# Performance work log

Measured on AMD Instinct MI355X. Metric: run time of the kernel, lower is better.

The kernel has to match this reference:

```python
import jax, jax.numpy as jnp
import numpy as np

NUM_HEADS = 8

def _l2norm(t, eps=1e-12):
    # F.normalize(p=2, dim=-1) with eps clamp
    n = jnp.sqrt(jnp.sum(t * t, axis=-1, keepdims=True))
    return t / jnp.maximum(n, eps)

def setup_inputs() -> dict:
    key = jax.random.key(0)
    ks = jax.random.split(key, 4)
    B, N, C = 16, 3136, 768
    x = jax.random.normal(ks[0], (B, N, C), dtype=jnp.float32)
    W_qkv = jax.random.normal(ks[1], (C, 3 * C), dtype=jnp.float32) * (1.0 / np.sqrt(C))
    temp = jnp.ones((NUM_HEADS, 1, 1), dtype=jnp.float32)
    W_proj = jax.random.normal(ks[2], (C, C), dtype=jnp.float32) * (1.0 / np.sqrt(C))
    b_proj = jnp.zeros((C,), dtype=jnp.float32)
    return {"x": x, "W_qkv": W_qkv, "temp": temp, "W_proj": W_proj, "b_proj": b_proj}

def reference(x, W_qkv, temp, W_proj, b_proj):
    B, N, C = x.shape
    h = NUM_HEADS
    d = C // h
    qkv = (x @ W_qkv).reshape(B, N, 3, h, d)
    qkv = jnp.transpose(qkv, (2, 0, 3, 1, 4))  # [3,B,h,N,d]
    q, k, v = qkv[0], qkv[1], qkv[2]           # [B,h,N,d]
    # transpose to channel-major: [B,h,d,N]
    q = jnp.swapaxes(q, -2, -1)
    k = jnp.swapaxes(k, -2, -1)
    v = jnp.swapaxes(v, -2, -1)
    q = _l2norm(q)
    k = _l2norm(k)
    # attn = k @ q^T over token dim: [B,h,d,d]
    attn = jnp.einsum('bhcn,bhen->bhce', k, q)
    attn = attn * temp  # temp broadcasts [h,1,1]
    attn = jax.nn.softmax(attn, axis=-1)
    out = jnp.einsum('bhce,bhen->bhcn', attn, v)  # [B,h,d,N]
    out = jnp.transpose(out, (0, 3, 1, 2)).reshape(B, N, C)
    return out @ W_proj + b_proj
```

## Files before the change

### kernel.cpp

```cpp
#include <hip/hip_runtime.h>

using bf16x8 = __attribute__((ext_vector_type(8))) __bf16;
using f32x4  = __attribute__((ext_vector_type(4))) float;

#define AS1 __attribute__((address_space(1)))
#define AS3 __attribute__((address_space(3)))

__device__ __forceinline__ unsigned short f2bf(float f) {
    unsigned int x = __float_as_uint(f);
    x += 0x7fffu + ((x >> 16) & 1u);
    return (unsigned short)(x >> 16);
}

__device__ __forceinline__ int xcd_remap(int orig, int nwg) {
    int q = nwg >> 3, r = nwg & 7;
    int xcd = orig & 7, lin = orig >> 3;
    return (xcd < r ? xcd * (q + 1) : r * (q + 1) + (xcd - r) * q) + lin;
}

__global__ __launch_bounds__(256)
void prep_kernel(const float* __restrict__ x, ushort4* __restrict__ xbf,
                 const float* __restrict__ Wqkv, unsigned short* __restrict__ wqkvt,
                 const float* __restrict__ Wproj, unsigned short* __restrict__ wprojt) {
    __shared__ float tile[32][33];
    int bid = blockIdx.x, tid = threadIdx.x;
    if (bid < 1728 + 576) {
        const float* W; unsigned short* Wt; int K = 768, N; int bx, by;
        if (bid < 1728) { W = Wqkv; Wt = wqkvt; N = 2304; bx = bid % 72; by = bid / 72; }
        else            { int t = bid - 1728; W = Wproj; Wt = wprojt; N = 768; bx = t % 24; by = t / 24; }
        int n0 = bx << 5, k0 = by << 5;
        int tx = tid & 31, ty = tid >> 5;
#pragma unroll
        for (int i = 0; i < 32; i += 8)
            tile[ty + i][tx] = W[(size_t)(k0 + ty + i) * N + (n0 + tx)];
        __syncthreads();
#pragma unroll
        for (int i = 0; i < 32; i += 8)
            Wt[(size_t)(n0 + ty + i) * K + (k0 + tx)] = f2bf(tile[tx][ty + i]);
    } else {
        int vb = bid - 2304;
        const float4* in = (const float4*)x;
        int n4 = 38535168 / 4;
        int stride = 2048 * 256;
        for (int i = vb * 256 + tid; i < n4; i += stride) {
            float4 v = in[i];
            ushort4 o;
            o.x = f2bf(v.x); o.y = f2bf(v.y); o.z = f2bf(v.z); o.w = f2bf(v.w);
            xbf[i] = o;
        }
    }
}

__device__ __forceinline__ void stage_tile_128x64(const unsigned short* g, int ldK,
                                                  unsigned short* lds, int tid) {
#pragma unroll
    for (int r = 0; r < 4; ++r) {
        int i = (r << 8) + tid;
        int row = i >> 3;
        int colb = (i & 7) << 4;
        int srcb = row * (ldK << 1) + (colb ^ ((row & 7) << 4));
        __builtin_amdgcn_global_load_lds(
            (AS1 unsigned int*)(unsigned long long)((const char*)g + srcb),
            (AS3 unsigned int*)((char*)lds + (i << 4)),
            16, 0, 0);
    }
}

__device__ __forceinline__ bf16x8 lds_read_swz(const unsigned short* base, int row, int kbyte) {
    int off = (row << 7) + (kbyte ^ ((row & 7) << 4));
    return *(const bf16x8*)((const char*)base + off);
}

__global__ __launch_bounds__(256, 2)
void gemm_bt_kernel(const unsigned short* __restrict__ A, const unsigned short* __restrict__ Bt,
                    unsigned short* __restrict__ obf, int M, int N, int K, int ntx) {
    __shared__ unsigned short As[128 * 64];
    __shared__ unsigned short Bs[128 * 64];
    int tid = threadIdx.x;
    int lane = tid & 63, w = tid >> 6;
    int wm = w >> 1, wn = w & 1;
    int wg = xcd_remap(blockIdx.x, gridDim.x);
    int bx = wg % ntx, by = wg / ntx;
    int m0 = by << 7, n0 = bx << 7;
    const unsigned short* Ag = A + (size_t)m0 * K;
    const unsigned short* Bg = Bt + (size_t)n0 * K;

    f32x4 zz = {0.f, 0.f, 0.f, 0.f};
    f32x4 acc[4][4];
#pragma unroll
    for (int a = 0; a < 4; ++a)
#pragma unroll
        for (int b = 0; b < 4; ++b) acc[a][b] = zz;

    for (int kb = 0; kb < K; kb += 64) {
        stage_tile_128x64(Ag + kb, K, As, tid);
        stage_tile_128x64(Bg + kb, K, Bs, tid);
        __syncthreads();
#pragma unroll
        for (int ks = 0; ks < 2; ++ks) {
            int kbyte = (ks << 6) + ((lane >> 4) << 4);
            bf16x8 af[4], bfr[4];
#pragma unroll
            for (int f = 0; f < 4; ++f)
                af[f] = lds_read_swz(As, (wm << 6) + (f << 4) + (lane & 15), kbyte);
#pragma unroll
            for (int f = 0; f < 4; ++f)
                bfr[f] = lds_read_swz(Bs, (wn << 6) + (f << 4) + (lane & 15), kbyte);
#pragma unroll
            for (int fm = 0; fm < 4; ++fm)
#pragma unroll
                for (int fn = 0; fn < 4; ++fn)
                    acc[fm][fn] = __builtin_amdgcn_mfma_f32_16x16x32_bf16(af[fm], bfr[fn], acc[fm][fn], 0, 0, 0);
        }
        __syncthreads();
    }

    int rbase = m0 + (wm << 6) + ((lane >> 4) << 2);
    int cbase = n0 + (wn << 6) + (lane & 15);
#pragma unroll
    for (int fm = 0; fm < 4; ++fm)
#pragma unroll
        for (int j = 0; j < 4; ++j) {
            size_t ro = (size_t)(rbase + (fm << 4) + j) * N;
#pragma unroll
            for (int fn = 0; fn < 4; ++fn)
                obf[ro + cbase + (fn << 4)] = f2bf(acc[fm][fn][j]);
        }
}

__global__ __launch_bounds__(256, 2)
void gemm_v_proj_kernel(const unsigned short* __restrict__ qkv, const unsigned short* __restrict__ MT,
                        float* __restrict__ out, const float* __restrict__ bias) {
    __shared__ unsigned short As[128 * 64];
    __shared__ unsigned short Bs[128 * 64];
    int tid = threadIdx.x;
    int lane = tid & 63, w = tid >> 6;
    int wm = w >> 1, wn = w & 1;
    int wg = xcd_remap(blockIdx.x, gridDim.x);
    int bx = wg % 6;
    int t2 = wg / 6;
    int mt = t2 % 25, b = t2 / 25;
    int m0 = mt << 7, n0 = bx << 7;
    const unsigned short* Ab = qkv + (size_t)b * 3136 * 2304 + 1536;
    const unsigned short* Bg = MT + (size_t)b * 589824 + (size_t)n0 * 768;

    f32x4 zz = {0.f, 0.f, 0.f, 0.f};
    f32x4 acc[4][4];
#pragma unroll
    for (int a = 0; a < 4; ++a)
#pragma unroll
        for (int c = 0; c < 4; ++c) acc[a][c] = zz;

    for (int kb = 0; kb < 768; kb += 64) {
#pragma unroll
        for (int r = 0; r < 4; ++r) {
            int i = (r << 8) + tid;
            int row = i >> 3, slot = i & 7;
            int rg = m0 + row; if (rg > 3135) rg = 3135;
            const char* src = (const char*)(Ab + (size_t)rg * 2304 + kb) + ((slot ^ (row & 7)) << 4);
            __builtin_amdgcn_global_load_lds(
                (AS1 unsigned int*)(unsigned long long)src,
                (AS3 unsigned int*)((char*)As + (i << 4)), 16, 0, 0);
        }
        stage_tile_128x64(Bg + kb, 768, Bs, tid);
        __syncthreads();
#pragma unroll
        for (int ks = 0; ks < 2; ++ks) {
            int kbyte = (ks << 6) + ((lane >> 4) << 4);
            bf16x8 af[4], bfr[4];
#pragma unroll
            for (int f = 0; f < 4; ++f)
                af[f] = lds_read_swz(As, (wm << 6) + (f << 4) + (lane & 15), kbyte);
#pragma unroll
            for (int f = 0; f < 4; ++f)
                bfr[f] = lds_read_swz(Bs, (wn << 6) + (f << 4) + (lane & 15), kbyte);
#pragma unroll
            for (int fm = 0; fm < 4; ++fm)
#pragma unroll
                for (int fn = 0; fn < 4; ++fn)
                    acc[fm][fn] = __builtin_amdgcn_mfma_f32_16x16x32_bf16(af[fm], bfr[fn], acc[fm][fn], 0, 0, 0);
        }
        __syncthreads();
    }

    int rloc = m0 + (wm << 6) + ((lane >> 4) << 2);
    int cbase = n0 + (wn << 6) + (lane & 15);
    float bv[4];
#pragma unroll
    for (int fn = 0; fn < 4; ++fn) bv[fn] = bias[cbase + (fn << 4)];
#pragma unroll
    for (int fm = 0; fm < 4; ++fm)
#pragma unroll
        for (int j = 0; j < 4; ++j) {
            int rr = rloc + (fm << 4) + j;
            if (rr < 3136) {
                size_t ro = ((size_t)b * 3136 + rr) * 768;
#pragma unroll
                for (int fn = 0; fn < 4; ++fn)
                    out[ro + cbase + (fn << 4)] = acc[fm][fn][j] + bv[fn];
            }
        }
}

__global__ __launch_bounds__(256)
void cov_mfma_kernel(const unsigned short* __restrict__ qkv, float* __restrict__ S,
                     float* __restrict__ qn2, float* __restrict__ kn2) {
    __shared__ unsigned short Kl[96 * 40];
    __shared__ unsigned short Ql[96 * 40];
    int bh = blockIdx.x;
    int b = bh >> 3, h = bh & 7;
    int tok0 = blockIdx.y * 448;
    int tid = threadIdx.x;
    int lane = tid & 63, w = tid >> 6;
    int wr = w & 1, wc = w >> 1;
    int rot = tid & 7;

    f32x4 zz = {0.f, 0.f, 0.f, 0.f};
    f32x4 acc[3][3];
#pragma unroll
    for (int a = 0; a < 3; ++a)
#pragma unroll
        for (int c = 0; c < 3; ++c) acc[a][c] = zz;
    float qn = 0.f, kn = 0.f;

    const uint4* qg = (const uint4*)qkv;

    for (int step = 0; step < 14; ++step) {
        int tokBase = b * 3136 + tok0 + (step << 5);
        __syncthreads();
#pragma unroll
        for (int r = 0; r < 3; ++r) {
            int idx = (r << 8) + tid;
            int isK = idx >= 384;
            int j = isK ? idx - 384 : idx;
            int tok = j / 12, c = j % 12;
            uint4 u = qg[(size_t)(tokBase + tok) * 288 + h * 12 + (isK ? 96 : 0) + c];
            unsigned short* dst = isK ? Kl : Ql;
            const unsigned short* us = (const unsigned short*)&u;
#pragma unroll
            for (int i = 0; i < 8; ++i) {
                int e = (i + rot) & 7;
                dst[(c * 8 + e) * 40 + tok] = us[e];
            }
        }
        __syncthreads();
        if (tid < 96) {
#pragma unroll
            for (int t = 0; t < 4; ++t) {
                bf16x8 v = *(const bf16x8*)((const char*)Ql + tid * 80 + (t << 4));
#pragma unroll
                for (int i = 0; i < 8; ++i) { float f = (float)v[i]; qn = fmaf(f, f, qn); }
            }
        } else if (tid >= 128 && tid < 224) {
            int c = tid - 128;
#pragma unroll
            for (int t = 0; t < 4; ++t) {
                bf16x8 v = *(const bf16x8*)((const char*)Kl + c * 80 + (t << 4));
#pragma unroll
                for (int i = 0; i < 8; ++i) { float f = (float)v[i]; kn = fmaf(f, f, kn); }
            }
        }
        int kbyte = (lane >> 4) << 4;
        bf16x8 af[3], bfv[3];
#pragma unroll
        for (int f = 0; f < 3; ++f)
            af[f] = *(const bf16x8*)((const char*)Kl + (wr * 48 + f * 16 + (lane & 15)) * 80 + kbyte);
#pragma unroll
        for (int f = 0; f < 3; ++f)
            bfv[f] = *(const bf16x8*)((const char*)Ql + (wc * 48 + f * 16 + (lane & 15)) * 80 + kbyte);
#pragma unroll
        for (int fm = 0; fm < 3; ++fm)
#pragma unroll
            for (int fn = 0; fn < 3; ++fn)
                acc[fm][fn] = __builtin_amdgcn_mfma_f32_16x16x32_bf16(af[fm], bfv[fn], acc[fm][fn], 0, 0, 0);
    }

    float* Sb = S + (size_t)bh * 9216;
    int rloc = wr * 48 + ((lane >> 4) << 2);
    int cloc = wc * 48 + (lane & 15);
#pragma unroll
    for (int fm = 0; fm < 3; ++fm)
#pragma unroll
        for (int fn = 0; fn < 3; ++fn)
#pragma unroll
            for (int j = 0; j < 4; ++j)
                atomicAdd(&Sb[(rloc + fm * 16 + j) * 96 + cloc + fn * 16], acc[fm][fn][j]);
    if (tid < 96) atomicAdd(&qn2[bh * 96 + tid], qn);
    if (tid >= 128 && tid < 224) atomicAdd(&kn2[bh * 96 + tid - 128], kn);
}

__global__ __launch_bounds__(128)
void softmax_kernel(const float* __restrict__ S, const float* __restrict__ qn2,
                    const float* __restrict__ kn2, const float* __restrict__ temp,
                    unsigned short* __restrict__ attnT) {
    int bh = blockIdx.x, h = bh & 7;
    __shared__ float Sl[96 * 97];
    __shared__ float qinv[96];
    int tid = threadIdx.x;
    const float* Sg = S + (size_t)bh * 9216;
    for (int i = tid; i < 9216; i += 128) Sl[(i / 96) * 97 + (i % 96)] = Sg[i];
    if (tid < 96) qinv[tid] = 1.f / fmaxf(sqrtf(qn2[bh * 96 + tid]), 1e-12f);
    __syncthreads();
    if (tid < 96) {
        int c = tid;
        float scale = (1.f / fmaxf(sqrtf(kn2[bh * 96 + c]), 1e-12f)) * temp[h];
        float* row = &Sl[c * 97];
        float mx = -3.4e38f;
        for (int e = 0; e < 96; ++e) {
            float v = row[e] * scale * qinv[e];
            row[e] = v;
            mx = fmaxf(mx, v);
        }
        float s = 0.f;
        for (int e = 0; e < 96; ++e) {
            float p = __expf(row[e] - mx);
            row[e] = p;
            s += p;
        }
        float inv = 1.f / s;
        unsigned short* ab = attnT + (size_t)bh * 9216;
        for (int e = 0; e < 96; ++e) ab[e * 96 + c] = f2bf(row[e] * inv);
    }
}

__global__ __launch_bounds__(256)
void attn_M_kernel(const unsigned short* __restrict__ attnT, const unsigned short* __restrict__ wprojt,
                   unsigned short* __restrict__ MT) {
    int bh = blockIdx.x >> 2, oc = blockIdx.x & 3;
    int b = bh >> 3, h = bh & 7;
    int tid = threadIdx.x, lane = tid & 63, w = tid >> 6;
    int o0 = oc * 192 + w * 48;
    const unsigned short* At = attnT + (size_t)bh * 9216;

    f32x4 zz = {0.f, 0.f, 0.f, 0.f};
    f32x4 acc[6][3];
#pragma unroll
    for (int f = 0; f < 6; ++f)
#pragma unroll
        for (int g = 0; g < 3; ++g) acc[f][g] = zz;

#pragma unroll
    for (int ks = 0; ks < 3; ++ks) {
        int koff = ks * 32 + ((lane >> 4) << 3);
        bf16x8 a[6], bb[3];
#pragma unroll
        for (int f = 0; f < 6; ++f)
            a[f] = *(const bf16x8*)(At + (size_t)(f * 16 + (lane & 15)) * 96 + koff);
#pragma unroll
        for (int g = 0; g < 3; ++g)
            bb[g] = *(const bf16x8*)(wprojt + (size_t)(o0 + g * 16 + (lane & 15)) * 768 + h * 96 + koff);
#pragma unroll
        for (int f = 0; f < 6; ++f)
#pragma unroll
            for (int g = 0; g < 3; ++g)
                acc[f][g] = __builtin_amdgcn_mfma_f32_16x16x32_bf16(a[f], bb[g], acc[f][g], 0, 0, 0);
    }

#pragma unroll
    for (int f = 0; f < 6; ++f)
#pragma unroll
        for (int g = 0; g < 3; ++g) {
            int e = f * 16 + ((lane >> 4) << 2);
            int o = o0 + g * 16 + (lane & 15);
            ushort4 pk;
            pk.x = f2bf(acc[f][g][0]); pk.y = f2bf(acc[f][g][1]);
            pk.z = f2bf(acc[f][g][2]); pk.w = f2bf(acc[f][g][3]);
            *(ushort4*)&MT[((size_t)b * 768 + o) * 768 + h * 96 + e] = pk;
        }
}

extern "C" void kernel_launch(void* const* d_in, const int* in_sizes, int n_in,
                              void* d_out, int out_size, void* d_ws, size_t ws_size,
                              hipStream_t stream) {
    const float* x     = (const float*)d_in[0];
    const float* Wqkv  = (const float*)d_in[1];
    const float* temp  = (const float*)d_in[2];
    const float* Wproj = (const float*)d_in[3];
    const float* bproj = (const float*)d_in[4];
    float* out = (float*)d_out;
    char* ws = (char*)d_ws;

    unsigned short* xbf    = (unsigned short*)(ws);
    unsigned short* qkvbf  = (unsigned short*)(ws + 77070336);
    unsigned short* wqkvt  = (unsigned short*)(ws + 308281344);
    unsigned short* wprojt = (unsigned short*)(ws + 311820288);
    float*          Sbuf   = (float*)        (ws + 312999936);
    float*          qn2    = (float*)        (ws + 317718528);
    float*          kn2    = (float*)        (ws + 317767680);
    unsigned short* attnT  = (unsigned short*)(ws + 317816832);
    unsigned short* MT     = xbf;

    hipMemsetAsync(Sbuf, 0, 4718592 + 49152 + 49152, stream);

    prep_kernel<<<4352, 256, 0, stream>>>(x, (ushort4*)xbf, Wqkv, wqkvt, Wproj, wprojt);

    gemm_bt_kernel<<<392 * 18, 256, 0, stream>>>(xbf, wqkvt, qkvbf, 50176, 2304, 768, 18);
    cov_mfma_kernel<<<dim3(128, 7), 256, 0, stream>>>(qkvbf, Sbuf, qn2, kn2);
    softmax_kernel<<<128, 128, 0, stream>>>(Sbuf, qn2, kn2, temp, attnT);
    attn_M_kernel<<<512, 256, 0, stream>>>(attnT, wprojt, MT);
    gemm_v_proj_kernel<<<2400, 256, 0, stream>>>(qkvbf, MT, out, bproj);
}
```

Baseline: 405.0 us.

## Fuse softmax with attn-M GEMM, fold memset into prep, prefetch cov loads

Merges the softmax and attn_M kernels so the attention matrix stays in LDS instead of round-tripping through global memory, removing one launch. Zeroing of the accumulation buffers moves into extra prep_kernel blocks, replacing hipMemsetAsync. The covariance kernel register-prefetches the next step's Q/K tile while the current one is written to LDS, and the QKV GEMM epilogue uses nontemporal stores. The fused kernel runs only 128 blocks, each looping over all four output chunks, so the M computation gets less parallelism than the previous 512 blocks.

```diff
diff --git a/kernel.cpp b/kernel.cpp
--- a/kernel.cpp
+++ b/kernel.cpp
@@ -21,10 +21,11 @@
 __global__ __launch_bounds__(256)
 void prep_kernel(const float* __restrict__ x, ushort4* __restrict__ xbf,
                  const float* __restrict__ Wqkv, unsigned short* __restrict__ wqkvt,
-                 const float* __restrict__ Wproj, unsigned short* __restrict__ wprojt) {
+                 const float* __restrict__ Wproj, unsigned short* __restrict__ wprojt,
+                 float4* __restrict__ zbase) {
     __shared__ float tile[32][33];
     int bid = blockIdx.x, tid = threadIdx.x;
-    if (bid < 1728 + 576) {
+    if (bid < 2304) {
         const float* W; unsigned short* Wt; int K = 768, N; int bx, by;
         if (bid < 1728) { W = Wqkv; Wt = wqkvt; N = 2304; bx = bid % 72; by = bid / 72; }
         else            { int t = bid - 1728; W = Wproj; Wt = wprojt; N = 768; bx = t % 24; by = t / 24; }
@@ -37,7 +38,7 @@
 #pragma unroll
         for (int i = 0; i < 32; i += 8)
             Wt[(size_t)(n0 + ty + i) * K + (k0 + tx)] = f2bf(tile[tx][ty + i]);
-    } else {
+    } else if (bid < 4352) {
         int vb = bid - 2304;
         const float4* in = (const float4*)x;
         int n4 = 38535168 / 4;
@@ -48,6 +49,10 @@
             o.x = f2bf(v.x); o.y = f2bf(v.y); o.z = f2bf(v.z); o.w = f2bf(v.w);
             xbf[i] = o;
         }
+    } else {
+        int z = bid - 4352;
+        float4 zz4 = {0.f, 0.f, 0.f, 0.f};
+        for (int i = z * 256 + tid; i < 301056; i += 294 * 256) zbase[i] = zz4;
     }
 }
 
@@ -124,7 +129,7 @@
             size_t ro = (size_t)(rbase + (fm << 4) + j) * N;
 #pragma unroll
             for (int fn = 0; fn < 4; ++fn)
-                obf[ro + cbase + (fn << 4)] = f2bf(acc[fm][fn][j]);
+                __builtin_nontemporal_store(f2bf(acc[fm][fn][j]), &obf[ro + cbase + (fn << 4)]);
         }
 }
 
@@ -225,22 +230,45 @@
 
     const uint4* qg = (const uint4*)qkv;
 
-    for (int step = 0; step < 14; ++step) {
-        int tokBase = b * 3136 + tok0 + (step << 5);
-        __syncthreads();
+    int idx0 = tid;
+    uint4 u[3];
+    {
+        int tokBase = b * 3136 + tok0;
 #pragma unroll
         for (int r = 0; r < 3; ++r) {
-            int idx = (r << 8) + tid;
+            int idx = (r << 8) + idx0;
             int isK = idx >= 384;
             int j = isK ? idx - 384 : idx;
             int tok = j / 12, c = j % 12;
-            uint4 u = qg[(size_t)(tokBase + tok) * 288 + h * 12 + (isK ? 96 : 0) + c];
+            u[r] = qg[(size_t)(tokBase + tok) * 288 + h * 12 + (isK ? 96 : 0) + c];
+        }
+    }
+
+    for (int step = 0; step < 14; ++step) {
+        __syncthreads();
+#pragma unroll
+        for (int r = 0; r < 3; ++r) {
+            int idx = (r << 8) + idx0;
+            int isK = idx >= 384;
+            int j = isK ? idx - 384 : idx;
+            int tok = j / 12, c = j % 12;
             unsigned short* dst = isK ? Kl : Ql;
-            const unsigned short* us = (const unsigned short*)&u;
+            const unsigned short* us = (const unsigned short*)&u[r];
 #pragma unroll
             for (int i = 0; i < 8; ++i) {
                 int e = (i + rot) & 7;
                 dst[(c * 8 + e) * 40 + tok] = us[e];
+            }
+        }
+        if (step < 13) {
+            int tokBase = b * 3136 + tok0 + ((step + 1) << 5);
+#pragma unroll
+            for (int r = 0; r < 3; ++r) {
+                int idx = (r << 8) + idx0;
+                int isK = idx >= 384;
+                int j = isK ? idx - 384 : idx;
+                int tok = j / 12, c = j % 12;
+                u[r] = qg[(size_t)(tokBase + tok) * 288 + h * 12 + (isK ? 96 : 0) + c];
             }
         }
         __syncthreads();
@@ -289,16 +317,18 @@
     if (tid >= 128 && tid < 224) atomicAdd(&kn2[bh * 96 + tid - 128], kn);
 }
 
-__global__ __launch_bounds__(128)
-void softmax_kernel(const float* __restrict__ S, const float* __restrict__ qn2,
-                    const float* __restrict__ kn2, const float* __restrict__ temp,
-                    unsigned short* __restrict__ attnT) {
-    int bh = blockIdx.x, h = bh & 7;
+__global__ __launch_bounds__(256)
+void softmax_M_kernel(const float* __restrict__ S, const float* __restrict__ qn2,
+                      const float* __restrict__ kn2, const float* __restrict__ temp,
+                      const unsigned short* __restrict__ wprojt, unsigned short* __restrict__ MT) {
+    int bh = blockIdx.x, h = bh & 7, b = bh >> 3;
     __shared__ float Sl[96 * 97];
     __shared__ float qinv[96];
-    int tid = threadIdx.x;
+    __shared__ unsigned short At[96 * 96];
+    int tid = threadIdx.x, lane = tid & 63, w = tid >> 6;
+    int l15 = lane & 15;
     const float* Sg = S + (size_t)bh * 9216;
-    for (int i = tid; i < 9216; i += 128) Sl[(i / 96) * 97 + (i % 96)] = Sg[i];
+    for (int i = tid; i < 9216; i += 256) Sl[(i / 96) * 97 + (i % 96)] = Sg[i];
     if (tid < 96) qinv[tid] = 1.f / fmaxf(sqrtf(qn2[bh * 96 + tid]), 1e-12f);
     __syncthreads();
     if (tid < 96) {
@@ -318,55 +348,46 @@
             s += p;
         }
         float inv = 1.f / s;
-        unsigned short* ab = attnT + (size_t)bh * 9216;
-        for (int e = 0; e < 96; ++e) ab[e * 96 + c] = f2bf(row[e] * inv);
-    }
-}
-
-__global__ __launch_bounds__(256)
-void attn_M_kernel(const unsigned short* __restrict__ attnT, const unsigned short* __restrict__ wprojt,
-                   unsigned short* __restrict__ MT) {
-    int bh = blockIdx.x >> 2, oc = blockIdx.x & 3;
-    int b = bh >> 3, h = bh & 7;
-    int tid = threadIdx.x, lane = tid & 63, w = tid >> 6;
-    int o0 = oc * 192 + w * 48;
-    const unsigned short* At = attnT + (size_t)bh * 9216;
+        for (int e = 0; e < 96; ++e) At[e * 96 + c] = f2bf(row[e] * inv);
+    }
+    __syncthreads();
 
     f32x4 zz = {0.f, 0.f, 0.f, 0.f};
-    f32x4 acc[6][3];
-#pragma unroll
-    for (int f = 0; f < 6; ++f)
-#pragma unroll
-        for (int g = 0; g < 3; ++g) acc[f][g] = zz;
-
-#pragma unroll
-    for (int ks = 0; ks < 3; ++ks) {
-        int koff = ks * 32 + ((lane >> 4) << 3);
-        bf16x8 a[6], bb[3];
+    for (int oc = 0; oc < 4; ++oc) {
+        int o0 = oc * 192 + w * 48;
+        f32x4 acc[6][3];
 #pragma unroll
         for (int f = 0; f < 6; ++f)
-            a[f] = *(const bf16x8*)(At + (size_t)(f * 16 + (lane & 15)) * 96 + koff);
-#pragma unroll
-        for (int g = 0; g < 3; ++g)
-            bb[g] = *(const bf16x8*)(wprojt + (size_t)(o0 + g * 16 + (lane & 15)) * 768 + h * 96 + koff);
+#pragma unroll
+            for (int g = 0; g < 3; ++g) acc[f][g] = zz;
+#pragma unroll
+        for (int ks = 0; ks < 3; ++ks) {
+            int koff = ks * 32 + ((lane >> 4) << 3);
+            bf16x8 a[6], bb[3];
+#pragma unroll
+            for (int f = 0; f < 6; ++f)
+                a[f] = *(const bf16x8*)(At + (f * 16 + l15) * 96 + koff);
+#pragma unroll
+            for (int g = 0; g < 3; ++g)
+                bb[g] = *(const bf16x8*)(wprojt + (size_t)(o0 + g * 16 + l15) * 768 + h * 96 + koff);
+#pragma unroll
+            for (int f = 0; f < 6; ++f)
+#pragma unroll
+                for (int g = 0; g < 3; ++g)
+                    acc[f][g] = __builtin_amdgcn_mfma_f32_16x16x32_bf16(a[f], bb[g], acc[f][g], 0, 0, 0);
+        }
 #pragma unroll
         for (int f = 0; f < 6; ++f)
 #pragma unroll
-            for (int g = 0; g < 3; ++g)
-                acc[f][g] = __builtin_amdgcn_mfma_f32_16x16x32_bf16(a[f], bb[g], acc[f][g], 0, 0, 0);
-    }
-
-#pragma unroll
-    for (int f = 0; f < 6; ++f)
-#pragma unroll
-        for (int g = 0; g < 3; ++g) {
-            int e = f * 16 + ((lane >> 4) << 2);
-            int o = o0 + g * 16 + (lane & 15);
-            ushort4 pk;
-            pk.x = f2bf(acc[f][g][0]); pk.y = f2bf(acc[f][g][1]);
-            pk.z = f2bf(acc[f][g][2]); pk.w = f2bf(acc[f][g][3]);
-            *(ushort4*)&MT[((size_t)b * 768 + o) * 768 + h * 96 + e] = pk;
-        }
+            for (int g = 0; g < 3; ++g) {
+                int e = f * 16 + ((lane >> 4) << 2);
+                int o = o0 + g * 16 + l15;
+                ushort4 pk;
+                pk.x = f2bf(acc[f][g][0]); pk.y = f2bf(acc[f][g][1]);
+                pk.z = f2bf(acc[f][g][2]); pk.w = f2bf(acc[f][g][3]);
+                *(ushort4*)&MT[((size_t)b * 768 + o) * 768 + h * 96 + e] = pk;
+            }
+    }
 }
 
 extern "C" void kernel_launch(void* const* d_in, const int* in_sizes, int n_in,
@@ -387,16 +408,13 @@
     float*          Sbuf   = (float*)        (ws + 312999936);
     float*          qn2    = (float*)        (ws + 317718528);
     float*          kn2    = (float*)        (ws + 317767680);
-    unsigned short* attnT  = (unsigned short*)(ws + 317816832);
     unsigned short* MT     = xbf;
 
-    hipMemsetAsync(Sbuf, 0, 4718592 + 49152 + 49152, stream);
-
-    prep_kernel<<<4352, 256, 0, stream>>>(x, (ushort4*)xbf, Wqkv, wqkvt, Wproj, wprojt);
+    prep_kernel<<<4646, 256, 0, stream>>>(x, (ushort4*)xbf, Wqkv, wqkvt, Wproj, wprojt,
+                                          (float4*)Sbuf);
 
     gemm_bt_kernel<<<392 * 18, 256, 0, stream>>>(xbf, wqkvt, qkvbf, 50176, 2304, 768, 18);
     cov_mfma_kernel<<<dim3(128, 7), 256, 0, stream>>>(qkvbf, Sbuf, qn2, kn2);
-    softmax_kernel<<<128, 128, 0, stream>>>(Sbuf, qn2, kn2, temp, attnT);
-    attn_M_kernel<<<512, 256, 0, stream>>>(attnT, wprojt, MT);
+    softmax_M_kernel<<<128, 256, 0, stream>>>(Sbuf, qn2, kn2, temp, wprojt, MT);
     gemm_v_proj_kernel<<<2400, 256, 0, stream>>>(qkvbf, MT, out, bproj);
 }
```

Result: slower. 422.2 us (+4.2%).
